# Performance work log

Hardware: AMD Instinct MI355X
Metric: run time of the kernel (lower is better)

## Reference

```python
import jax, jax.numpy as jnp
import numpy as np
import math

D = 1024
B, S = 4, 2048


def setup_inputs() -> dict:
    key = jax.random.key(0)
    ks = jax.random.split(key, 16)
    sc = 0.02
    def lin(k, dout, din):
        kw, kb = jax.random.split(k)
        return (sc * jax.random.normal(kw, (dout, din), jnp.float32),
                sc * jax.random.normal(kb, (dout,), jnp.float32))
    Wq, bq = lin(ks[0], D, D)
    Wk, bk = lin(ks[1], D, D)
    Wv, bv = lin(ks[2], D, D)
    Wmu, bmu = lin(ks[3], D, D)
    Wlv, blv = lin(ks[4], D, D)
    Wg, bg = lin(ks[5], 1, D)
    gamma = jnp.ones((D,), jnp.float32)
    beta = jnp.zeros((D,), jnp.float32)
    x = jax.random.normal(ks[6], (B, S, D), jnp.float32)
    eps = jax.random.normal(ks[7], (B, S, D), jnp.float32)
    return dict(x=x, eps=eps, Wq=Wq, bq=bq, Wk=Wk, bk=bk, Wv=Wv, bv=bv,
                Wmu=Wmu, bmu=bmu, Wlv=Wlv, blv=blv, Wg=Wg, bg=bg,
                gamma=gamma, beta=beta)


def _layernorm(x, gamma, beta, eps=1e-5):
    mu = jnp.mean(x, axis=-1, keepdims=True)
    var = jnp.mean(jnp.square(x - mu), axis=-1, keepdims=True)
    return (x - mu) * jax.lax.rsqrt(var + eps) * gamma + beta


def reference(x, eps, Wq, bq, Wk, bk, Wv, bv, Wmu, bmu, Wlv, blv, Wg, bg, gamma, beta):
    d = x.shape[-1]
    Q = jnp.einsum('bsd,ed->bse', x, Wq) + bq
    K = jnp.einsum('bsd,ed->bse', x, Wk) + bk
    V = jnp.einsum('bsd,ed->bse', x, Wv) + bv
    scores = jnp.einsum('bqd,bkd->bqk', Q, K) / (math.sqrt(d) * 1.5)
    attn = jax.nn.softmax(scores, axis=-1)
    h = jnp.einsum('bqk,bkd->bqd', attn, V)
    mu = jnp.einsum('bsd,ed->bse', h, Wmu) + bmu
    logvar = jnp.einsum('bsd,ed->bse', h, Wlv) + blv
    std = jnp.exp(0.5 * logvar)
    z = jax.nn.relu(mu + eps * std)
    p_gate = jax.nn.sigmoid(jnp.einsum('bd,ed->be', h.mean(axis=1), Wg) + bg)
    out = _layernorm(x + z, gamma, beta)
    return out, mu, logvar, p_gate.squeeze(-1)
```

## Files before the change

### kernel.cpp

```cpp
#include <hip/hip_runtime.h>

typedef unsigned short u16;
typedef __attribute__((ext_vector_type(8))) short bf16x8;
typedef __attribute__((ext_vector_type(4))) float f32x4;

__device__ inline float bf2f(u16 h) {
    union { unsigned u; float f; } v; v.u = ((unsigned)h) << 16; return v.f;
}
__device__ inline u16 f2bf(float f) {
    union { float f; unsigned u; } v; v.f = f;
    unsigned r = v.u + 0x7fffu + ((v.u >> 16) & 1u);
    return (u16)(r >> 16);
}

__device__ inline void gl_lds16(const u16* g, u16* l) {
    __builtin_amdgcn_global_load_lds(
        (const __attribute__((address_space(1))) void*)g,
        (__attribute__((address_space(3))) void*)l, 16, 0, 0);
}

__device__ __forceinline__ void wgbar() {
    asm volatile("" ::: "memory");
    __builtin_amdgcn_s_barrier();
    asm volatile("" ::: "memory");
}
#define VMW(n) asm volatile("s_waitcnt vmcnt(" #n ")" ::: "memory")

__global__ __launch_bounds__(256) void cvt_bf16_k(
    const float* __restrict__ s0, u16* __restrict__ d0, long long n0,
    const float* __restrict__ s1, u16* __restrict__ d1, long long n1,
    const float* __restrict__ s2, u16* __restrict__ d2, long long n2,
    const float* __restrict__ s3, u16* __restrict__ d3, long long n3)
{
    int y = blockIdx.y;
    const float* s = (y == 0) ? s0 : (y == 1) ? s1 : (y == 2) ? s2 : s3;
    u16* d         = (y == 0) ? d0 : (y == 1) ? d1 : (y == 2) ? d2 : d3;
    long long n    = (y == 0) ? n0 : (y == 1) ? n1 : (y == 2) ? n2 : n3;
    for (long long i = (long long)blockIdx.x * 256 + threadIdx.x; i < n;
         i += (long long)gridDim.x * 256) {
        float4 v = ((const float4*)s)[i];
        union { u16 h[4]; unsigned long long u; } p;
        p.h[0] = f2bf(v.x); p.h[1] = f2bf(v.y);
        p.h[2] = f2bf(v.z); p.h[3] = f2bf(v.w);
        ((unsigned long long*)d)[i] = p.u;
    }
}

#define OSTA(T, SL2, S)                                                       \
    { const u16* g_ = Ag + (long long)((S) * 64 + w * 16 + orow) * K          \
                      + (long long)(T) * 32 + oscol;                          \
      gl_lds16(g_, &As[SL2][(S) * 2048 + w * 512]); }

#define OSTB(T, SL2, S)                                                       \
    { const u16* g_ = Bg + (long long)(bn0 + (S) * 64 + w * 16 + orow) * ldb  \
                      + (long long)(T) * 32 + oscol;                          \
      gl_lds16(g_, &Bs[SL2][(S) * 2048 + w * 512]); }

template <int COUTF32, int BIASROW, int NSPLIT, int NFAST>
__global__ __launch_bounds__(256, 3) void gemm_o(
    const u16* __restrict__ A, const u16* __restrict__ Bt,
    const float* __restrict__ bias0, const float* __restrict__ bias1,
    void* __restrict__ C0, void* __restrict__ C1,
    int M, int N, int K, int ldb, float scale,
    long long sAb, long long sBb, long long sCb, long long bofs_stride)
{
    __shared__ u16 As[3][4096];
    __shared__ u16 Bs[3][4096];

    int gx = gridDim.x, gy = gridDim.y;
    int n = gx * gy * gridDim.z;
    int flat = (blockIdx.z * gy + blockIdx.y) * gx + blockIdx.x;
    int L = (flat & 7) * (n >> 3) + (flat >> 3);
    int bz = L / (gx * gy);
    int rr = L - bz * gx * gy;
    int bx, by;
    if (NFAST) { bx = rr / gy; by = rr - bx * gy; }
    else       { by = rr / gx; bx = rr - by * gx; }

    int bm0 = bx * 128;
    int bn0 = by * 128;
    int b   = bz;
    int tid = threadIdx.x;
    int w = tid >> 6, l = tid & 63;
    int wm = w >> 1;
    int wn = w & 1;
    int lane15 = l & 15, quad = l >> 4;
    int xr = (l & 3) << 3;

    int orow  = l >> 2;
    int oscol = ((l & 3) ^ (orow & 3)) * 8;

    const u16* Ag = A  + (long long)b * sAb + (long long)bm0 * K;
    const u16* Bg = Bt + (long long)b * sBb + (long long)(bm0 >> 11) * bofs_stride;

    f32x4 acc[4][4];
#pragma unroll
    for (int i = 0; i < 4; i++)
#pragma unroll
        for (int j = 0; j < 4; j++) acc[i][j] = (f32x4)(0.0f);

    int NT = K >> 5;

    OSTA(0, 0, 0); OSTA(0, 0, 1); OSTB(0, 0, 0); OSTB(0, 0, 1);
    OSTA(1, 1, 0); OSTA(1, 1, 1); OSTB(1, 1, 0); OSTB(1, 1, 1);
    VMW(4);
    wgbar();

    int sl = 0, sl2 = 2;
    for (int t = 0; t < NT; ++t) {
        bf16x8 av[4], bvv[4];
#pragma unroll
        for (int ii = 0; ii < 4; ii++)
            av[ii] = *(const bf16x8*)&As[sl][
                (wm * 64 + ii * 16 + lane15) * 32 + ((quad * 8) ^ xr)];
#pragma unroll
        for (int jj = 0; jj < 4; jj++)
            bvv[jj] = *(const bf16x8*)&Bs[sl][
                (wn * 64 + jj * 16 + lane15) * 32 + ((quad * 8) ^ xr)];

        if (t + 2 < NT) {
            int t2 = t + 2;
            OSTA(t2, sl2, 0); OSTA(t2, sl2, 1);
            OSTB(t2, sl2, 0); OSTB(t2, sl2, 1);
            VMW(4);
        } else if (t + 1 < NT) {
            VMW(0);
        }
        wgbar();

        __builtin_amdgcn_s_setprio(1);
#pragma unroll
        for (int ii = 0; ii < 4; ii++)
#pragma unroll
            for (int jj = 0; jj < 4; jj++)
                acc[ii][jj] = __builtin_amdgcn_mfma_f32_16x16x32_bf16(
                    av[ii], bvv[jj], acc[ii][jj], 0, 0, 0);
        __builtin_amdgcn_s_setprio(0);
        wgbar();

        sl  = (sl  == 2) ? 0 : sl + 1;
        sl2 = (sl2 == 2) ? 0 : sl2 + 1;
    }

    float rowb_[4][4];
    if (BIASROW) {
#pragma unroll
        for (int i = 0; i < 4; i++)
#pragma unroll
            for (int r = 0; r < 4; r++)
                rowb_[i][r] = bias0[bm0 + wm * 64 + i * 16 + quad * 4 + r];
    }
#pragma unroll
    for (int jj = 0; jj < 4; jj++) {
        int col = bn0 + wn * 64 + jj * 16 + lane15;
        int seg, cl, cstride;
        if (NSPLIT == 1) { seg = 0; cl = col; cstride = N; }
        else             { seg = col >> 10; cl = col & 1023; cstride = 1024; }
        const float* bp = (seg == 0) ? bias0 : bias1;
        void* cb = (seg == 0) ? C0 : C1;
        u16*   c16 = (u16*)cb   + (long long)b * sCb;
        float* c32 = (float*)cb + (long long)b * sCb;
        float bvc = (!BIASROW && bp) ? bp[cl] : 0.0f;
#pragma unroll
        for (int i = 0; i < 4; i++) {
            int row0 = bm0 + wm * 64 + i * 16 + quad * 4;
#pragma unroll
            for (int r = 0; r < 4; r++) {
                float v = acc[i][jj][r] * scale + (BIASROW ? rowb_[i][r] : bvc);
                if (COUTF32) c32[(long long)(row0 + r) * cstride + cl] = v;
                else         c16[(long long)(row0 + r) * cstride + cl] = f2bf(v);
            }
        }
    }
}

__global__ __launch_bounds__(256) void softmax_k(u16* __restrict__ Sc)
{
    long long row = blockIdx.x;
    u16* s = Sc + row * 2048;
    int t = threadIdx.x;

    uint4 raw = *(const uint4*)(s + t * 8);
    const u16* rp = (const u16*)&raw;
    float v[8];
    float mx = -3.4e38f;
#pragma unroll
    for (int j = 0; j < 8; j++) { v[j] = bf2f(rp[j]); mx = fmaxf(mx, v[j]); }
#pragma unroll
    for (int o = 32; o > 0; o >>= 1) mx = fmaxf(mx, __shfl_xor(mx, o));
    __shared__ float redm[4];
    if ((t & 63) == 0) redm[t >> 6] = mx;
    __syncthreads();
    mx = fmaxf(fmaxf(redm[0], redm[1]), fmaxf(redm[2], redm[3]));

    float sum = 0.0f;
#pragma unroll
    for (int j = 0; j < 8; j++) { v[j] = __expf(v[j] - mx); sum += v[j]; }
#pragma unroll
    for (int o = 32; o > 0; o >>= 1) sum += __shfl_xor(sum, o);
    __shared__ float reds[4];
    if ((t & 63) == 0) reds[t >> 6] = sum;
    __syncthreads();
    sum = reds[0] + reds[1] + reds[2] + reds[3];

    float inv = 1.0f / sum;
    u16 o8[8];
#pragma unroll
    for (int j = 0; j < 8; j++) o8[j] = f2bf(v[j] * inv);
    *(uint4*)(s + t * 8) = *(const uint4*)o8;
}

__global__ __launch_bounds__(256) void gate_partial(const u16* __restrict__ h,
                                                    const float* __restrict__ Wg,
                                                    float* __restrict__ part)
{
    int b = blockIdx.x, c = blockIdx.y;
    int t = threadIdx.x;
    int tx = t & 127;
    int ty = t >> 7;
    int d0 = tx * 8;
    const u16* hb = h + (long long)b * 2048 * 1024 + (long long)c * 16 * 1024;

    float wg[8];
#pragma unroll
    for (int j = 0; j < 8; j++) wg[j] = Wg[d0 + j];

    float acc = 0.0f;
    for (int s = ty; s < 16; s += 2) {
        bf16x8 hv = *(const bf16x8*)&hb[(long long)s * 1024 + d0];
        const u16* hp = (const u16*)&hv;
#pragma unroll
        for (int j = 0; j < 8; j++) acc += bf2f(hp[j]) * wg[j];
    }
#pragma unroll
    for (int o = 32; o > 0; o >>= 1) acc += __shfl_xor(acc, o);
    __shared__ float red[4];
    if ((t & 63) == 0) red[t >> 6] = acc;
    __syncthreads();
    if (t == 0) part[b * 128 + c] = red[0] + red[1] + red[2] + red[3];
}

__global__ void gate_final(const float* __restrict__ part,
                           const float* __restrict__ bg, float* __restrict__ outp)
{
    int t = threadIdx.x;
    if (t < 4) {
        float s = 0.0f;
        for (int c = 0; c < 128; c++) s += part[t * 128 + c];
        float v = s * (1.0f / 2048.0f) + bg[0];
        outp[t] = 1.0f / (1.0f + __expf(-v));
    }
}

__global__ __launch_bounds__(256) void epilogue_k(
    const float* __restrict__ x, const float* __restrict__ ep,
    const float* __restrict__ mu, const float* __restrict__ lv,
    const float* __restrict__ gamma, const float* __restrict__ beta,
    float* __restrict__ out)
{
    long long base = (long long)blockIdx.x * 1024;
    int t = threadIdx.x;
    int i0 = t * 4;

    float4 xv = *(const float4*)&x[base + i0];
    float4 ev = *(const float4*)&ep[base + i0];
    float4 mv = *(const float4*)&mu[base + i0];
    float4 lw = *(const float4*)&lv[base + i0];

    float y[4];
    y[0] = xv.x + fmaxf(mv.x + ev.x * __expf(0.5f * lw.x), 0.0f);
    y[1] = xv.y + fmaxf(mv.y + ev.y * __expf(0.5f * lw.y), 0.0f);
    y[2] = xv.z + fmaxf(mv.z + ev.z * __expf(0.5f * lw.z), 0.0f);
    y[3] = xv.w + fmaxf(mv.w + ev.w * __expf(0.5f * lw.w), 0.0f);

    float sum = 0.0f, sq = 0.0f;
#pragma unroll
    for (int j = 0; j < 4; j++) { sum += y[j]; sq += y[j] * y[j]; }
#pragma unroll
    for (int o = 32; o > 0; o >>= 1) { sum += __shfl_xor(sum, o); sq += __shfl_xor(sq, o); }
    __shared__ float rs[4], rq[4];
    if ((t & 63) == 0) { rs[t >> 6] = sum; rq[t >> 6] = sq; }
    __syncthreads();
    sum = rs[0] + rs[1] + rs[2] + rs[3];
    sq  = rq[0] + rq[1] + rq[2] + rq[3];
    float mean = sum * (1.0f / 1024.0f);
    float var  = fmaxf(sq * (1.0f / 1024.0f) - mean * mean, 0.0f);
    float rstd = rsqrtf(var + 1e-5f);

    float4 gv = *(const float4*)&gamma[i0];
    float4 bv = *(const float4*)&beta[i0];
    float4 o;
    o.x = (y[0] - mean) * rstd * gv.x + bv.x;
    o.y = (y[1] - mean) * rstd * gv.y + bv.y;
    o.z = (y[2] - mean) * rstd * gv.z + bv.z;
    o.w = (y[3] - mean) * rstd * gv.w + bv.w;
    *(float4*)&out[base + i0] = o;
}

extern "C" void kernel_launch(void* const* d_in, const int* in_sizes, int n_in,
                              void* d_out, int out_size, void* d_ws, size_t ws_size,
                              hipStream_t stream)
{
    const float* x     = (const float*)d_in[0];
    const float* ep    = (const float*)d_in[1];
    const float* Wq    = (const float*)d_in[2];
    const float* bq    = (const float*)d_in[3];
    const float* Wk    = (const float*)d_in[4];
    const float* bk    = (const float*)d_in[5];
    const float* Wv    = (const float*)d_in[6];
    const float* bv    = (const float*)d_in[7];
    const float* Wmu   = (const float*)d_in[8];
    const float* bmu   = (const float*)d_in[9];
    const float* Wlv   = (const float*)d_in[10];
    const float* blv   = (const float*)d_in[11];
    const float* Wg    = (const float*)d_in[12];
    const float* bg    = (const float*)d_in[13];
    const float* gamma = (const float*)d_in[14];
    const float* beta  = (const float*)d_in[15];
    float* out = (float*)d_out;

    const int M = 8192;
    const int D = 1024;
    const int S = 2048;

    float* mu_out = out + 8388608LL;
    float* lv_out = out + 16777216LL;
    float* pg_out = out + 25165824LL;

    u16* xb   = (u16*)out;
    u16* Wqb  = (u16*)out + 8388608LL;
    u16* Wkb  = (u16*)out + 9437184LL;
    u16* Wvb  = (u16*)out + 10485760LL;
    u16* Sc   = (u16*)out;
    u16* Q    = (u16*)mu_out;
    u16* Kb   = (u16*)mu_out + 8388608LL;
    u16* Vt   = (u16*)lv_out;
    u16* h    = (u16*)d_ws;
    float* part = (float*)out;
    u16* Wmub = (u16*)out + 2097152LL;
    u16* Wlvb = (u16*)out + 3145728LL;

    dim3 blk(256);

    cvt_bf16_k<<<dim3(2048, 4), blk, 0, stream>>>(
        x,  xb,  2097152LL,
        Wq, Wqb, 262144LL,
        Wk, Wkb, 262144LL,
        Wv, Wvb, 262144LL);

    gemm_o<0, 0, 2, 1><<<dim3(64, 16, 1), blk, 0, stream>>>(
        xb, Wqb, bq, bk, Q, Kb,
        M, 2048, D, D, 1.0f, 0, 0, 0, 0);

    gemm_o<0, 1, 1, 0><<<dim3(8, 64, 1), blk, 0, stream>>>(
        Wvb, xb, bv, nullptr, Vt, nullptr,
        D, 8192, D, D, 1.0f, 0, 0, 0, 0);

    gemm_o<0, 0, 1, 1><<<dim3(16, 16, 4), blk, 0, stream>>>(
        Q, Kb, nullptr, nullptr, Sc, nullptr,
        S, S, D, D, 1.0f / 48.0f,
        (long long)S * D, (long long)S * D, (long long)S * S, 0);

    softmax_k<<<dim3(8192), blk, 0, stream>>>(Sc);

    gemm_o<0, 0, 1, 1><<<dim3(64, 8, 1), blk, 0, stream>>>(
        Sc, Vt, nullptr, nullptr, h, nullptr,
        M, D, S, 8192, 1.0f, 0, 0, 0, 2048);

    cvt_bf16_k<<<dim3(512, 2), blk, 0, stream>>>(
        Wmu, Wmub, 262144LL,
        Wlv, Wlvb, 262144LL,
        nullptr, nullptr, 0LL,
        nullptr, nullptr, 0LL);

    gemm_o<1, 0, 2, 1><<<dim3(64, 16, 1), blk, 0, stream>>>(
        h, Wmub, bmu, blv, (void*)mu_out, (void*)lv_out,
        M, 2048, D, D, 1.0f, 0, 0, 0, 0);

    gate_partial<<<dim3(4, 128), blk, 0, stream>>>(h, Wg, part);
    gate_final<<<dim3(1), dim3(64), 0, stream>>>(part, bg, pg_out);

    epilogue_k<<<dim3(8192), blk, 0, stream>>>(x, ep, mu_out, lv_out, gamma, beta, out);
}
```

Before: 417.0 us.

## Merge QKV GEMMs into one launch and fuse gate reduction into PV epilogue

The Q/K projection GEMM and the transposed V projection GEMM now run as a single kernel launch, with the block index choosing which body to execute. This is meant to fill the GPU better and remove one launch gap. The gate mean is now accumulated in the epilogue of the attention-times-V GEMM using atomics, and the sigmoid runs inside the final epilogue kernel, which removes two small kernels and one extra read of h. The atomic accumulation adds a non-deterministic summation order and an extra syncthreads in the GEMM epilogue.

After: 407.4 us. 2.3% less time.

```diff
diff --git a/kernel.cpp b/kernel.cpp
--- a/kernel.cpp
+++ b/kernel.cpp
@@ -49,38 +49,30 @@
 #define OSTA(T, SL2, S)                                                       \
     { const u16* g_ = Ag + (long long)((S) * 64 + w * 16 + orow) * K          \
                       + (long long)(T) * 32 + oscol;                          \
-      gl_lds16(g_, &As[SL2][(S) * 2048 + w * 512]); }
+      gl_lds16(g_, &As[(SL2) * 4096 + (S) * 2048 + w * 512]); }
 
 #define OSTB(T, SL2, S)                                                       \
     { const u16* g_ = Bg + (long long)(bn0 + (S) * 64 + w * 16 + orow) * ldb  \
                       + (long long)(T) * 32 + oscol;                          \
-      gl_lds16(g_, &Bs[SL2][(S) * 2048 + w * 512]); }
-
-template <int COUTF32, int BIASROW, int NSPLIT, int NFAST>
-__global__ __launch_bounds__(256, 3) void gemm_o(
+      gl_lds16(g_, &Bs[(SL2) * 4096 + (S) * 2048 + w * 512]); }
+
+template <int COUTF32, int BIASROW, int NSPLIT, int GATE>
+__device__ __forceinline__ void gemm_body(
     const u16* __restrict__ A, const u16* __restrict__ Bt,
     const float* __restrict__ bias0, const float* __restrict__ bias1,
     void* __restrict__ C0, void* __restrict__ C1,
     int M, int N, int K, int ldb, float scale,
-    long long sAb, long long sBb, long long sCb, long long bofs_stride)
-{
-    __shared__ u16 As[3][4096];
-    __shared__ u16 Bs[3][4096];
-
-    int gx = gridDim.x, gy = gridDim.y;
-    int n = gx * gy * gridDim.z;
-    int flat = (blockIdx.z * gy + blockIdx.y) * gx + blockIdx.x;
-    int L = (flat & 7) * (n >> 3) + (flat >> 3);
-    int bz = L / (gx * gy);
-    int rr = L - bz * gx * gy;
-    int bx, by;
-    if (NFAST) { bx = rr / gy; by = rr - bx * gy; }
-    else       { by = rr / gx; bx = rr - by * gx; }
+    long long sAb, long long sBb, long long sCb, long long bofs_stride,
+    int bx, int by, int bz, int tid,
+    const float* __restrict__ Wg, float* __restrict__ gatebuf,
+    u16* lds)
+{
+    u16* As = lds;
+    u16* Bs = lds + 12288;
 
     int bm0 = bx * 128;
     int bn0 = by * 128;
     int b   = bz;
-    int tid = threadIdx.x;
     int w = tid >> 6, l = tid & 63;
     int wm = w >> 1;
     int wn = w & 1;
@@ -111,11 +103,11 @@
         bf16x8 av[4], bvv[4];
 #pragma unroll
         for (int ii = 0; ii < 4; ii++)
-            av[ii] = *(const bf16x8*)&As[sl][
+            av[ii] = *(const bf16x8*)&As[sl * 4096 +
                 (wm * 64 + ii * 16 + lane15) * 32 + ((quad * 8) ^ xr)];
 #pragma unroll
         for (int jj = 0; jj < 4; jj++)
-            bvv[jj] = *(const bf16x8*)&Bs[sl][
+            bvv[jj] = *(const bf16x8*)&Bs[sl * 4096 +
                 (wn * 64 + jj * 16 + lane15) * 32 + ((quad * 8) ^ xr)];
 
         if (t + 2 < NT) {
@@ -150,6 +142,7 @@
             for (int r = 0; r < 4; r++)
                 rowb_[i][r] = bias0[bm0 + wm * 64 + i * 16 + quad * 4 + r];
     }
+    float gsum = 0.0f;
 #pragma unroll
     for (int jj = 0; jj < 4; jj++) {
         int col = bn0 + wn * 64 + jj * 16 + lane15;
@@ -161,24 +154,91 @@
         u16*   c16 = (u16*)cb   + (long long)b * sCb;
         float* c32 = (float*)cb + (long long)b * sCb;
         float bvc = (!BIASROW && bp) ? bp[cl] : 0.0f;
+        float wgc = GATE ? Wg[cl] : 0.0f;
 #pragma unroll
         for (int i = 0; i < 4; i++) {
             int row0 = bm0 + wm * 64 + i * 16 + quad * 4;
 #pragma unroll
             for (int r = 0; r < 4; r++) {
                 float v = acc[i][jj][r] * scale + (BIASROW ? rowb_[i][r] : bvc);
+                if (GATE) gsum += v * wgc;
                 if (COUTF32) c32[(long long)(row0 + r) * cstride + cl] = v;
                 else         c16[(long long)(row0 + r) * cstride + cl] = f2bf(v);
             }
         }
     }
-}
-
-__global__ __launch_bounds__(256) void softmax_k(u16* __restrict__ Sc)
+    if (GATE) {
+#pragma unroll
+        for (int o = 32; o > 0; o >>= 1) gsum += __shfl_xor(gsum, o);
+        float* red = (float*)lds;
+        __syncthreads();
+        if ((tid & 63) == 0) red[tid >> 6] = gsum;
+        __syncthreads();
+        if (tid == 0)
+            atomicAdd(&gatebuf[bm0 >> 11],
+                      red[0] + red[1] + red[2] + red[3]);
+    }
+}
+
+template <int COUTF32, int BIASROW, int NSPLIT, int NFAST, int GATE>
+__global__ __launch_bounds__(256, 3) void gemm_o(
+    const u16* __restrict__ A, const u16* __restrict__ Bt,
+    const float* __restrict__ bias0, const float* __restrict__ bias1,
+    void* __restrict__ C0, void* __restrict__ C1,
+    int M, int N, int K, int ldb, float scale,
+    long long sAb, long long sBb, long long sCb, long long bofs_stride,
+    const float* __restrict__ Wg, float* __restrict__ gatebuf)
+{
+    __shared__ u16 lds[24576];
+
+    int gx = gridDim.x, gy = gridDim.y;
+    int n = gx * gy * gridDim.z;
+    int flat = (blockIdx.z * gy + blockIdx.y) * gx + blockIdx.x;
+    int L = (flat & 7) * (n >> 3) + (flat >> 3);
+    int bz = L / (gx * gy);
+    int rr = L - bz * gx * gy;
+    int bx, by;
+    if (NFAST) { bx = rr / gy; by = rr - bx * gy; }
+    else       { by = rr / gx; bx = rr - by * gx; }
+
+    gemm_body<COUTF32, BIASROW, NSPLIT, GATE>(
+        A, Bt, bias0, bias1, C0, C1, M, N, K, ldb, scale,
+        sAb, sBb, sCb, bofs_stride, bx, by, bz, threadIdx.x, Wg, gatebuf, lds);
+}
+
+__global__ __launch_bounds__(256, 3) void qkv_k(
+    const u16* __restrict__ xb, const u16* __restrict__ Wqb,
+    const float* __restrict__ bq, const float* __restrict__ bk,
+    u16* __restrict__ Q, u16* __restrict__ Kb,
+    const u16* __restrict__ Wvb, const float* __restrict__ bv,
+    u16* __restrict__ Vt)
+{
+    __shared__ u16 lds[24576];
+    int flat = blockIdx.x;
+    int tid = threadIdx.x;
+    if (flat < 1024) {
+        int L = (flat & 7) * 128 + (flat >> 3);
+        int bx = L / 16, by = L - bx * 16;
+        gemm_body<0, 0, 2, 0>(
+            xb, Wqb, bq, bk, Q, Kb, 8192, 2048, 1024, 1024, 1.0f,
+            0, 0, 0, 0, bx, by, 0, tid, nullptr, nullptr, lds);
+    } else {
+        int f2 = flat - 1024;
+        int L = (f2 & 7) * 64 + (f2 >> 3);
+        int by = L / 8, bx = L - by * 8;
+        gemm_body<0, 1, 1, 0>(
+            Wvb, xb, bv, nullptr, Vt, nullptr, 1024, 8192, 1024, 1024, 1.0f,
+            0, 0, 0, 0, bx, by, 0, tid, nullptr, nullptr, lds);
+    }
+}
+
+__global__ __launch_bounds__(256) void softmax_k(u16* __restrict__ Sc,
+                                                 float* __restrict__ gatebuf)
 {
     long long row = blockIdx.x;
     u16* s = Sc + row * 2048;
     int t = threadIdx.x;
+    if (blockIdx.x == 0 && t < 4) gatebuf[t] = 0.0f;
 
     uint4 raw = *(const uint4*)(s + t * 8);
     const u16* rp = (const u16*)&raw;
@@ -210,57 +270,20 @@
     *(uint4*)(s + t * 8) = *(const uint4*)o8;
 }
 
-__global__ __launch_bounds__(256) void gate_partial(const u16* __restrict__ h,
-                                                    const float* __restrict__ Wg,
-                                                    float* __restrict__ part)
-{
-    int b = blockIdx.x, c = blockIdx.y;
-    int t = threadIdx.x;
-    int tx = t & 127;
-    int ty = t >> 7;
-    int d0 = tx * 8;
-    const u16* hb = h + (long long)b * 2048 * 1024 + (long long)c * 16 * 1024;
-
-    float wg[8];
-#pragma unroll
-    for (int j = 0; j < 8; j++) wg[j] = Wg[d0 + j];
-
-    float acc = 0.0f;
-    for (int s = ty; s < 16; s += 2) {
-        bf16x8 hv = *(const bf16x8*)&hb[(long long)s * 1024 + d0];
-        const u16* hp = (const u16*)&hv;
-#pragma unroll
-        for (int j = 0; j < 8; j++) acc += bf2f(hp[j]) * wg[j];
-    }
-#pragma unroll
-    for (int o = 32; o > 0; o >>= 1) acc += __shfl_xor(acc, o);
-    __shared__ float red[4];
-    if ((t & 63) == 0) red[t >> 6] = acc;
-    __syncthreads();
-    if (t == 0) part[b * 128 + c] = red[0] + red[1] + red[2] + red[3];
-}
-
-__global__ void gate_final(const float* __restrict__ part,
-                           const float* __restrict__ bg, float* __restrict__ outp)
-{
-    int t = threadIdx.x;
-    if (t < 4) {
-        float s = 0.0f;
-        for (int c = 0; c < 128; c++) s += part[t * 128 + c];
-        float v = s * (1.0f / 2048.0f) + bg[0];
-        outp[t] = 1.0f / (1.0f + __expf(-v));
-    }
-}
-
 __global__ __launch_bounds__(256) void epilogue_k(
     const float* __restrict__ x, const float* __restrict__ ep,
     const float* __restrict__ mu, const float* __restrict__ lv,
     const float* __restrict__ gamma, const float* __restrict__ beta,
-    float* __restrict__ out)
+    float* __restrict__ out, const float* __restrict__ bg,
+    float* __restrict__ pg)
 {
     long long base = (long long)blockIdx.x * 1024;
     int t = threadIdx.x;
     int i0 = t * 4;
+    if (blockIdx.x == 0 && t < 4) {
+        float v = pg[t] * (1.0f / 2048.0f) + bg[0];
+        pg[t] = 1.0f / (1.0f + __expf(-v));
+    }
 
     float4 xv = *(const float4*)&x[base + i0];
     float4 ev = *(const float4*)&ep[base + i0];
@@ -336,7 +359,6 @@
     u16* Kb   = (u16*)mu_out + 8388608LL;
     u16* Vt   = (u16*)lv_out;
     u16* h    = (u16*)d_ws;
-    float* part = (float*)out;
     u16* Wmub = (u16*)out + 2097152LL;
     u16* Wlvb = (u16*)out + 3145728LL;
 
@@ -348,24 +370,21 @@
         Wk, Wkb, 262144LL,
         Wv, Wvb, 262144LL);
 
-    gemm_o<0, 0, 2, 1><<<dim3(64, 16, 1), blk, 0, stream>>>(
-        xb, Wqb, bq, bk, Q, Kb,
-        M, 2048, D, D, 1.0f, 0, 0, 0, 0);
-
-    gemm_o<0, 1, 1, 0><<<dim3(8, 64, 1), blk, 0, stream>>>(
-        Wvb, xb, bv, nullptr, Vt, nullptr,
-        D, 8192, D, D, 1.0f, 0, 0, 0, 0);
-
-    gemm_o<0, 0, 1, 1><<<dim3(16, 16, 4), blk, 0, stream>>>(
+    qkv_k<<<dim3(1536), blk, 0, stream>>>(
+        xb, Wqb, bq, bk, Q, Kb, Wvb, bv, Vt);
+
+    gemm_o<0, 0, 1, 1, 0><<<dim3(16, 16, 4), blk, 0, stream>>>(
         Q, Kb, nullptr, nullptr, Sc, nullptr,
         S, S, D, D, 1.0f / 48.0f,
-        (long long)S * D, (long long)S * D, (long long)S * S, 0);
-
-    softmax_k<<<dim3(8192), blk, 0, stream>>>(Sc);
-
-    gemm_o<0, 0, 1, 1><<<dim3(64, 8, 1), blk, 0, stream>>>(
+        (long long)S * D, (long long)S * D, (long long)S * S, 0,
+        nullptr, nullptr);
+
+    softmax_k<<<dim3(8192), blk, 0, stream>>>(Sc, pg_out);
+
+    gemm_o<0, 0, 1, 1, 1><<<dim3(64, 8, 1), blk, 0, stream>>>(
         Sc, Vt, nullptr, nullptr, h, nullptr,
-        M, D, S, 8192, 1.0f, 0, 0, 0, 2048);
+        M, D, S, 8192, 1.0f, 0, 0, 0, 2048,
+        Wg, pg_out);
 
     cvt_bf16_k<<<dim3(512, 2), blk, 0, stream>>>(
         Wmu, Wmub, 262144LL,
@@ -373,12 +392,11 @@
         nullptr, nullptr, 0LL,
         nullptr, nullptr, 0LL);
 
-    gemm_o<1, 0, 2, 1><<<dim3(64, 16, 1), blk, 0, stream>>>(
+    gemm_o<1, 0, 2, 1, 0><<<dim3(64, 16, 1), blk, 0, stream>>>(
         h, Wmub, bmu, blv, (void*)mu_out, (void*)lv_out,
-        M, 2048, D, D, 1.0f, 0, 0, 0, 0);
-
-    gate_partial<<<dim3(4, 128), blk, 0, stream>>>(h, Wg, part);
-    gate_final<<<dim3(1), dim3(64), 0, stream>>>(part, bg, pg_out);
-
-    epilogue_k<<<dim3(8192), blk, 0, stream>>>(x, ep, mu_out, lv_out, gamma, beta, out);
-}
+        M, 2048, D, D, 1.0f, 0, 0, 0, 0,
+        nullptr, nullptr);
+
+    epilogue_k<<<dim3(8192), blk, 0, stream>>>(
+        x, ep, mu_out, lv_out, gamma, beta, out, bg, pg_out);
+}
```
